# Optimization experiments

Measured on AMD Instinct MI355X. Metric: run time of the kernel, lower is better.

## Reference

```python
import jax, jax.numpy as jnp
import numpy as np

N_QUBITS = 12
N_LAYERS = 6
BATCH = 512
DIM = 2 ** N_QUBITS


def _apply_1q(psi, G, wire):
    """Apply a single-qubit gate on `wire` (wire 0 = most significant).
    psi: [B, 2^n] complex. G: [2,2] (shared) or [B,2,2] (batched)."""
    B = psi.shape[0]
    left = 2 ** wire
    psi = psi.reshape(B, left, 2, -1)
    if G.ndim == 2:
        psi = jnp.einsum('ij,bxjy->bxiy', G, psi)
    else:
        psi = jnp.einsum('bij,bxjy->bxiy', G, psi)
    return psi.reshape(B, -1)


def _apply_cnot(psi, c, t):
    """CNOT with control c, target t on [B, 2^n] state."""
    B = psi.shape[0]
    ps = psi.reshape((B,) + (2,) * N_QUBITS)
    ca, ta = c + 1, t + 1
    c0 = jnp.take(ps, 0, axis=ca)
    c1 = jnp.take(ps, 1, axis=ca)
    flip_ax = ta if ta < ca else ta - 1
    c1 = jnp.flip(c1, axis=flip_ax)  # X on target within control=1 block
    ps = jnp.stack([c0, c1], axis=ca)
    return ps.reshape(B, -1)


def _circuit(x, weights):
    B = x.shape[0]
    psi = jnp.zeros((B, DIM), jnp.complex64).at[:, 0].set(1.0)

    # AngleEmbedding: RY(x_w) on each wire (batched gate matrices)
    h = 0.5 * x
    c, s = jnp.cos(h).astype(jnp.complex64), jnp.sin(h).astype(jnp.complex64)
    for w in range(N_QUBITS):
        G = jnp.stack([jnp.stack([c[:, w], -s[:, w]], -1),
                       jnp.stack([s[:, w], c[:, w]], -1)], -2)  # [B,2,2]
        psi = _apply_1q(psi, G, w)

    # StronglyEntanglingLayers: Rot(phi,theta,omega) per wire, then ring of CNOTs
    for l in range(N_LAYERS):
        phi, theta, omega = weights[l, :, 0], weights[l, :, 1], weights[l, :, 2]
        ct = jnp.cos(0.5 * theta).astype(jnp.complex64)
        st = jnp.sin(0.5 * theta).astype(jnp.complex64)
        ep = jnp.exp(-0.5j * (phi + omega).astype(jnp.complex64))
        em = jnp.exp(0.5j * (phi - omega).astype(jnp.complex64))
        # Rot = RZ(omega) RY(theta) RZ(phi)
        m00 = ep * ct
        m01 = -em * st
        m10 = jnp.conj(em) * st
        m11 = jnp.conj(ep) * ct
        for w in range(N_QUBITS):
            G = jnp.array([[m00[w], m01[w]], [m10[w], m11[w]]], jnp.complex64)
            psi = _apply_1q(psi, G, w)
        r = l % (N_QUBITS - 1) + 1
        for w in range(N_QUBITS):
            psi = _apply_cnot(psi, w, (w + r) % N_QUBITS)

    # <Z_w> for every wire
    probs = psi.real ** 2 + psi.imag ** 2  # [B, 2^n]
    exps = []
    for w in range(N_QUBITS):
        p = probs.reshape(B, 2 ** w, 2, -1)
        exps.append(p[:, :, 0, :].sum((1, 2)) - p[:, :, 1, :].sum((1, 2)))
    return jnp.stack(exps, -1)  # [B, n_qubits]


def setup_inputs() -> dict:
    key = jax.random.key(0)
    k1, k2, k3, k4 = jax.random.split(key, 4)
    x = jax.random.uniform(k1, (BATCH, N_QUBITS), jnp.float32, -np.pi, np.pi)
    weights = jax.random.uniform(k2, (N_LAYERS, N_QUBITS, 3), jnp.float32, 0.0, 2.0 * np.pi)
    W = jax.random.normal(k3, (1, N_QUBITS), jnp.float32) * 0.3
    b = jax.random.normal(k4, (1,), jnp.float32) * 0.01
    return {"x": x, "weights": weights, "W": W, "b": b}


def reference(x, weights, W, b):
    z = _circuit(x, weights)              # [B, n_qubits]
    y = z @ W.T + b                       # [B, 1]
    return y.squeeze(-1)                  # [B]
```

## Files before the change

kernel.cpp:

```cpp
#include <hip/hip_runtime.h>
#include <stdint.h>

#define NQ 12
#define DIM 4096
#define NLAYERS 6
#define TPB 256

struct CK_t {
    uint32_t RC1[NLAYERS][NQ];
    uint32_t RC2[NQ];
    uint32_t RC3[NQ];
    uint32_t frow[NQ];
};

constexpr uint32_t G2f(uint32_t k){ return ((k&15u)<<8) | (k&0xF0u) | ((k>>8)&15u); }
constexpr uint32_t G3f(uint32_t k){ return ((k&15u)<<4) | ((k>>4)&15u) | (k&0xF00u); }
constexpr uint32_t Lstd(uint32_t k){ return ((k&15u)<<8) | (k>>4); }
constexpr uint32_t Lpr(uint32_t k){ return ((k>>6)&15u) | (((k>>4)&3u)<<4) | (((k>>10)&3u)<<6) | ((k&15u)<<8); }

constexpr CK_t build_ck() {
    CK_t ck{};
    uint32_t Acols[NLAYERS][NQ]{}, Aicol5[NQ]{};
    for (int l = 0; l < NLAYERS; l++) {
        int r = l % (NQ - 1) + 1;
        for (int q = 0; q < NQ; q++) {
            uint32_t v = 1u << q;
            for (int w = NQ - 1; w >= 0; w--) {
                int pc = NQ - 1 - w, pt = NQ - 1 - ((w + r) % NQ);
                v ^= ((v >> pc) & 1u) << pt;
            }
            Acols[l][q] = v;
            if (l == NLAYERS - 1) {
                uint32_t u = 1u << q;
                for (int w = 0; w < NQ; w++) {
                    int pc = NQ - 1 - w, pt = NQ - 1 - ((w + r) % NQ);
                    u ^= ((u >> pc) & 1u) << pt;
                }
                Aicol5[q] = u;
            }
        }
    }
    for (int j = 0; j < NQ; j++) ck.RC2[j] = Lstd(G2f(1u << j));
    for (int j = 0; j < NQ; j++) ck.RC3[j] = Lpr(G3f(1u << j));
    for (int l = 1; l < NLAYERS; l++)
        for (int j = 0; j < NQ; j++)
            ck.RC1[l][j] = Lstd(G3f(G2f(Acols[l - 1][j])));
    uint32_t Mcol[NQ]{};
    for (int j = 0; j < NQ; j++) {
        uint32_t pj = G2f(G3f(1u << j));
        uint32_t M = 0;
        for (int m = 0; m < NQ; m++) if ((pj >> m) & 1u) M ^= Aicol5[m];
        Mcol[j] = M;
    }
    for (int p = 0; p < NQ; p++) {
        uint32_t s = 0;
        for (int j = 0; j < NQ; j++) s |= ((Mcol[j] >> p) & 1u) << j;
        ck.frow[p] = s;
    }
    return ck;
}
constexpr CK_t CK = build_ck();

template<int KIND, int L, int PAR>
__device__ __forceinline__ void do_pass(float (&RE)[16], float (&IM)[16],
                                        float2* xb, int tid) {
    float2* buf = xb + PAR * DIM;
    int wbase;
    if constexpr (KIND == 3) wbase = (int)Lpr((uint32_t)tid << 4);
    else                     wbase = tid;
    #pragma unroll
    for (int l = 0; l < 16; l++)
        buf[wbase + (l << 8)] = make_float2(RE[l], IM[l]);

    uint32_t srcT = 0;
    #pragma unroll
    for (int j = 0; j < 8; j++) {
        uint32_t c = (KIND == 1) ? CK.RC1[L][4 + j]
                   : (KIND == 2) ? CK.RC2[4 + j] : CK.RC3[4 + j];
        srcT ^= ((tid >> j) & 1) ? c : 0u;
    }
    __syncthreads();
    #pragma unroll
    for (int l = 0; l < 16; l++) {
        uint32_t C = 0;
        #pragma unroll
        for (int q = 0; q < 4; q++)
            if ((l >> q) & 1)
                C ^= (KIND == 1) ? CK.RC1[L][q]
                   : (KIND == 2) ? CK.RC2[q] : CK.RC3[q];
        float2 v = buf[srcT ^ C];
        RE[l] = v.x; IM[l] = v.y;
    }
}

template<int L, int W, int Q>
__device__ __forceinline__ void reg_gate(float (&RE)[16], float (&IM)[16],
                                         const float4* smat) {
    float4 m = smat[L * NQ + W];
    #pragma unroll
    for (int l = 0; l < 16; l++) {
        if (l & (1 << Q)) continue;
        int l2 = l | (1 << Q);
        float a0r = RE[l], a0i = IM[l], a1r = RE[l2], a1i = IM[l2];
        RE[l]  = m.x * a0r - m.y * a0i + m.z * a1r - m.w * a1i;
        IM[l]  = m.x * a0i + m.y * a0r + m.z * a1i + m.w * a1r;
        RE[l2] = m.x * a1r + m.y * a1i - m.z * a0r - m.w * a0i;
        IM[l2] = m.x * a1i - m.y * a1r - m.z * a0i + m.w * a0r;
    }
}

template<int L>
__device__ __forceinline__ void do_layer(float (&RE)[16], float (&IM)[16],
                                         const float4* smat, float2* xb, int tid) {
    if constexpr (L > 0)
        do_pass<1, L, (3 * L - 1) & 1>(RE, IM, xb, tid);
    reg_gate<L, 11, 0>(RE, IM, smat);
    reg_gate<L, 10, 1>(RE, IM, smat);
    reg_gate<L,  9, 2>(RE, IM, smat);
    reg_gate<L,  8, 3>(RE, IM, smat);
    do_pass<2, L, (3 * L) & 1>(RE, IM, xb, tid);
    reg_gate<L, 3, 0>(RE, IM, smat);
    reg_gate<L, 2, 1>(RE, IM, smat);
    reg_gate<L, 1, 2>(RE, IM, smat);
    reg_gate<L, 0, 3>(RE, IM, smat);
    do_pass<3, L, (3 * L + 1) & 1>(RE, IM, xb, tid);
    reg_gate<L, 7, 0>(RE, IM, smat);
    reg_gate<L, 6, 1>(RE, IM, smat);
    reg_gate<L, 5, 2>(RE, IM, smat);
    reg_gate<L, 4, 3>(RE, IM, smat);
}

__global__ __launch_bounds__(TPB) void qsim_kernel(
    const float* __restrict__ x,
    const float* __restrict__ weights,
    const float* __restrict__ Wp,
    const float* __restrict__ bptr,
    float* __restrict__ out)
{
    __shared__ float2 xb[2 * DIM];
    __shared__ float4 smat[NLAYERS * NQ];
    __shared__ float  scs[NQ], sss[NQ];
    __shared__ float  red[4];

    const int tid = threadIdx.x;
    const int b   = blockIdx.x;

    if (tid < NQ) {
        float s_, c_;
        sincosf(0.5f * x[b * NQ + tid], &s_, &c_);
        scs[tid] = c_; sss[tid] = s_;
    }
    if (tid < NLAYERS * NQ) {
        float phi   = weights[tid * 3 + 0];
        float theta = weights[tid * 3 + 1];
        float omega = weights[tid * 3 + 2];
        float st, ct; sincosf(0.5f * theta, &st, &ct);
        float sp, cp; sincosf(0.5f * (phi + omega), &sp, &cp);
        float sm, cm; sincosf(0.5f * (phi - omega), &sm, &cm);
        smat[tid] = make_float4(cp * ct, -sp * ct, -cm * st, -sm * st);
    }
    __syncthreads();

    float base = 1.0f;
    #pragma unroll
    for (int p = 4; p < NQ; p++) {
        int w = NQ - 1 - p;
        base *= ((tid >> (p - 4)) & 1) ? sss[w] : scs[w];
    }
    float RE[16], IM[16];
    #pragma unroll
    for (int l = 0; l < 16; l++) {
        float a = base;
        #pragma unroll
        for (int p = 0; p < 4; p++) {
            int w = NQ - 1 - p;
            a *= ((l >> p) & 1) ? sss[w] : scs[w];
        }
        RE[l] = a; IM[l] = 0.0f;
    }

    do_layer<0>(RE, IM, smat, xb, tid);
    do_layer<1>(RE, IM, smat, xb, tid);
    do_layer<2>(RE, IM, smat, xb, tid);
    do_layer<3>(RE, IM, smat, xb, tid);
    do_layer<4>(RE, IM, smat, xb, tid);
    do_layer<5>(RE, IM, smat, xb, tid);

    const float bv = bptr[0];
    float wb[NQ];
    #pragma unroll
    for (int p = 0; p < NQ; p++) {
        uint32_t row = CK.frow[p];
        int tp = __popc(tid & (int)(row >> 4)) & 1;
        float Wv = Wp[NQ - 1 - p];
        wb[p] = tp ? -Wv : Wv;
    }
    float acc = 0.0f;
    #pragma unroll
    for (int l = 0; l < 16; l++) {
        float coef = bv;
        #pragma unroll
        for (int p = 0; p < NQ; p++)
            coef += (__popc(l & (int)(CK.frow[p] & 15u)) & 1) ? -wb[p] : wb[p];
        acc += (RE[l] * RE[l] + IM[l] * IM[l]) * coef;
    }
    #pragma unroll
    for (int off = 32; off > 0; off >>= 1)
        acc += __shfl_down(acc, off, 64);
    if ((tid & 63) == 0) red[tid >> 6] = acc;
    __syncthreads();
    if (tid == 0) out[b] = red[0] + red[1] + red[2] + red[3];
}

extern "C" void kernel_launch(void* const* d_in, const int* in_sizes, int n_in,
                              void* d_out, int out_size, void* d_ws, size_t ws_size,
                              hipStream_t stream) {
    const float* x       = (const float*)d_in[0];
    const float* weights = (const float*)d_in[1];
    const float* W       = (const float*)d_in[2];
    const float* bptr    = (const float*)d_in[3];
    qsim_kernel<<<512, TPB, 0, stream>>>(x, weights, W, bptr, (float*)d_out);
}
```

Measured before the change: 98.81 us.

## Compute conflict-avoiding shared-memory permutation layouts at compile time; pack complex as float2

Replaces the hand-written shared-memory index maps with layouts generated at compile time by a GF(2) basis search. The search picks write and read address bases so that wavefront accesses spread across LDS banks on both the store and the load side of each transpose pass. Thread address offsets for write and read are packed into a single XOR accumulation. It also stores amplitudes as two-wide float vectors so the gate math can use packed FP32 ops. The cost is a more complex constexpr construction and possibly different register allocation.

```diff
diff --git a/kernel.cpp b/kernel.cpp
--- a/kernel.cpp
+++ b/kernel.cpp
@@ -6,17 +6,91 @@
 #define NLAYERS 6
 #define TPB 256
 
+typedef float v2f __attribute__((ext_vector_type(2)));
+
+struct Pass_t {
+    uint32_t WT[8];
+    uint32_t WL[16];
+    uint32_t RT[8];
+    uint32_t RL[16];
+};
 struct CK_t {
-    uint32_t RC1[NLAYERS][NQ];
-    uint32_t RC2[NQ];
-    uint32_t RC3[NQ];
+    Pass_t PG2, PG3;
+    Pass_t P1[NLAYERS];
     uint32_t frow[NQ];
 };
 
 constexpr uint32_t G2f(uint32_t k){ return ((k&15u)<<8) | (k&0xF0u) | ((k>>8)&15u); }
 constexpr uint32_t G3f(uint32_t k){ return ((k&15u)<<4) | ((k>>4)&15u) | (k&0xF00u); }
-constexpr uint32_t Lstd(uint32_t k){ return ((k&15u)<<8) | (k>>4); }
-constexpr uint32_t Lpr(uint32_t k){ return ((k>>6)&15u) | (((k>>4)&3u)<<4) | (((k>>10)&3u)<<6) | ((k&15u)<<8); }
+
+constexpr uint32_t ech_reduce(const uint32_t* v, int n, uint32_t x){
+    bool ch = true;
+    while (ch) {
+        ch = false;
+        for (int i = 0; i < n; i++)
+            if (v[i] && (x ^ v[i]) < x) { x ^= v[i]; ch = true; }
+    }
+    return x;
+}
+
+constexpr Pass_t build_pass(const uint32_t* Mc) {
+    Pass_t P{};
+    uint32_t rows[12]{}; int nr = 0;
+    {
+        uint32_t e1[4]{}, e2[4]{}; int n1 = 0, n2 = 0;
+        for (int step = 0; step < 4; step++) {
+            bool found = false;
+            for (int pc = 1; pc <= 3 && !found; pc++) {
+                for (int a = 0; a < 12 && !found; a++)
+                for (int b = (pc >= 2 ? a + 1 : 12); (pc >= 2 ? b < 12 : b == 12) && !found; b++)
+                for (int c = (pc == 3 ? b + 1 : 12); (pc == 3 ? c < 12 : c == 12) && !found; c++) {
+                    uint32_t m = (1u << a);
+                    if (pc >= 2) m |= (1u << b);
+                    if (pc == 3) m |= (1u << c);
+                    uint32_t v1 = (m >> 4) & 15u;
+                    uint32_t v2 = 0;
+                    for (int j = 0; j < 4; j++)
+                        v2 |= (uint32_t)(__builtin_popcount(m & Mc[4 + j]) & 1) << j;
+                    uint32_t r1 = ech_reduce(e1, n1, v1);
+                    uint32_t r2 = ech_reduce(e2, n2, v2);
+                    if (r1 && r2) {
+                        rows[nr++] = m; e1[n1++] = r1; e2[n2++] = r2; found = true;
+                    }
+                }
+            }
+            if (!found) { rows[nr] = 1u << (4 + nr); nr++; }
+        }
+    }
+    {
+        uint32_t ef[12]{}; int nf = 0;
+        for (int i = 0; i < nr; i++) {
+            uint32_t r = ech_reduce(ef, nf, rows[i]);
+            if (r) ef[nf++] = r;
+        }
+        for (uint32_t m = 1; m < 4096u && nr < 12; m++) {
+            uint32_t r = ech_reduce(ef, nf, m);
+            if (r) { rows[nr++] = m; ef[nf++] = r; }
+        }
+    }
+    uint32_t col[12]{}, rc[12]{};
+    for (int j = 0; j < 12; j++) {
+        uint32_t c = 0;
+        for (int i = 0; i < 12; i++) c |= (uint32_t)((rows[i] >> j) & 1u) << i;
+        col[j] = c;
+    }
+    for (int j = 0; j < 12; j++) {
+        uint32_t a = 0, mc = Mc[j];
+        for (int q = 0; q < 12; q++) if ((mc >> q) & 1u) a ^= col[q];
+        rc[j] = a;
+    }
+    for (int j = 0; j < 8; j++) { P.WT[j] = col[4 + j]; P.RT[j] = rc[4 + j]; }
+    for (int l = 0; l < 16; l++) {
+        uint32_t aw = 0, ar = 0;
+        for (int q = 0; q < 4; q++) if ((l >> q) & 1) { aw ^= col[q]; ar ^= rc[q]; }
+        P.WL[l] = aw; P.RL[l] = ar;
+    }
+    return P;
+}
 
 constexpr CK_t build_ck() {
     CK_t ck{};
@@ -40,11 +114,14 @@
             }
         }
     }
-    for (int j = 0; j < NQ; j++) ck.RC2[j] = Lstd(G2f(1u << j));
-    for (int j = 0; j < NQ; j++) ck.RC3[j] = Lpr(G3f(1u << j));
-    for (int l = 1; l < NLAYERS; l++)
-        for (int j = 0; j < NQ; j++)
-            ck.RC1[l][j] = Lstd(G3f(G2f(Acols[l - 1][j])));
+    uint32_t McG2[12]{}, McG3[12]{}, Mc1[12]{};
+    for (int j = 0; j < 12; j++) { McG2[j] = G2f(1u << j); McG3[j] = G3f(1u << j); }
+    ck.PG2 = build_pass(McG2);
+    ck.PG3 = build_pass(McG3);
+    for (int l = 1; l < NLAYERS; l++) {
+        for (int j = 0; j < 12; j++) Mc1[j] = G3f(G2f(Acols[l - 1][j]));
+        ck.P1[l] = build_pass(Mc1);
+    }
     uint32_t Mcol[NQ]{};
     for (int j = 0; j < NQ; j++) {
         uint32_t pj = G2f(G3f(1u << j));
@@ -62,72 +139,59 @@
 constexpr CK_t CK = build_ck();
 
 template<int KIND, int L, int PAR>
-__device__ __forceinline__ void do_pass(float (&RE)[16], float (&IM)[16],
-                                        float2* xb, int tid) {
-    float2* buf = xb + PAR * DIM;
-    int wbase;
-    if constexpr (KIND == 3) wbase = (int)Lpr((uint32_t)tid << 4);
-    else                     wbase = tid;
+__device__ __forceinline__ void do_pass(v2f (&Z)[16], v2f* xb, int tid) {
+    constexpr Pass_t P = (KIND == 1) ? CK.P1[L] : (KIND == 2) ? CK.PG2 : CK.PG3;
+    v2f* buf = xb + PAR * DIM;
+    uint32_t comb = 0;
+    #pragma unroll
+    for (int j = 0; j < 8; j++) {
+        uint32_t pk = P.WT[j] | (P.RT[j] << 16);
+        comb ^= (uint32_t)(-(int)((tid >> j) & 1)) & pk;
+    }
+    uint32_t wbase = comb & 0xFFFu, rbase = comb >> 16;
     #pragma unroll
     for (int l = 0; l < 16; l++)
-        buf[wbase + (l << 8)] = make_float2(RE[l], IM[l]);
-
-    uint32_t srcT = 0;
-    #pragma unroll
-    for (int j = 0; j < 8; j++) {
-        uint32_t c = (KIND == 1) ? CK.RC1[L][4 + j]
-                   : (KIND == 2) ? CK.RC2[4 + j] : CK.RC3[4 + j];
-        srcT ^= ((tid >> j) & 1) ? c : 0u;
-    }
+        buf[wbase ^ P.WL[l]] = Z[l];
     __syncthreads();
     #pragma unroll
-    for (int l = 0; l < 16; l++) {
-        uint32_t C = 0;
-        #pragma unroll
-        for (int q = 0; q < 4; q++)
-            if ((l >> q) & 1)
-                C ^= (KIND == 1) ? CK.RC1[L][q]
-                   : (KIND == 2) ? CK.RC2[q] : CK.RC3[q];
-        float2 v = buf[srcT ^ C];
-        RE[l] = v.x; IM[l] = v.y;
-    }
+    for (int l = 0; l < 16; l++)
+        Z[l] = buf[rbase ^ P.RL[l]];
 }
 
 template<int L, int W, int Q>
-__device__ __forceinline__ void reg_gate(float (&RE)[16], float (&IM)[16],
-                                         const float4* smat) {
+__device__ __forceinline__ void reg_gate(v2f (&Z)[16], const float4* smat) {
     float4 m = smat[L * NQ + W];
     #pragma unroll
     for (int l = 0; l < 16; l++) {
         if (l & (1 << Q)) continue;
         int l2 = l | (1 << Q);
-        float a0r = RE[l], a0i = IM[l], a1r = RE[l2], a1i = IM[l2];
-        RE[l]  = m.x * a0r - m.y * a0i + m.z * a1r - m.w * a1i;
-        IM[l]  = m.x * a0i + m.y * a0r + m.z * a1i + m.w * a1r;
-        RE[l2] = m.x * a1r + m.y * a1i - m.z * a0r - m.w * a0i;
-        IM[l2] = m.x * a1i - m.y * a1r - m.z * a0i + m.w * a0r;
+        v2f z0 = Z[l], z1 = Z[l2];
+        v2f j0 = { -z0.y, z0.x };
+        v2f j1 = { -z1.y, z1.x };
+        Z[l]  = m.x * z0 + m.y * j0 + m.z * z1 + m.w * j1;
+        Z[l2] = m.x * z1 - m.y * j1 - m.z * z0 + m.w * j0;
     }
 }
 
 template<int L>
-__device__ __forceinline__ void do_layer(float (&RE)[16], float (&IM)[16],
-                                         const float4* smat, float2* xb, int tid) {
+__device__ __forceinline__ void do_layer(v2f (&Z)[16], const float4* smat,
+                                         v2f* xb, int tid) {
     if constexpr (L > 0)
-        do_pass<1, L, (3 * L - 1) & 1>(RE, IM, xb, tid);
-    reg_gate<L, 11, 0>(RE, IM, smat);
-    reg_gate<L, 10, 1>(RE, IM, smat);
-    reg_gate<L,  9, 2>(RE, IM, smat);
-    reg_gate<L,  8, 3>(RE, IM, smat);
-    do_pass<2, L, (3 * L) & 1>(RE, IM, xb, tid);
-    reg_gate<L, 3, 0>(RE, IM, smat);
-    reg_gate<L, 2, 1>(RE, IM, smat);
-    reg_gate<L, 1, 2>(RE, IM, smat);
-    reg_gate<L, 0, 3>(RE, IM, smat);
-    do_pass<3, L, (3 * L + 1) & 1>(RE, IM, xb, tid);
-    reg_gate<L, 7, 0>(RE, IM, smat);
-    reg_gate<L, 6, 1>(RE, IM, smat);
-    reg_gate<L, 5, 2>(RE, IM, smat);
-    reg_gate<L, 4, 3>(RE, IM, smat);
+        do_pass<1, L, (3 * L - 1) & 1>(Z, xb, tid);
+    reg_gate<L, 11, 0>(Z, smat);
+    reg_gate<L, 10, 1>(Z, smat);
+    reg_gate<L,  9, 2>(Z, smat);
+    reg_gate<L,  8, 3>(Z, smat);
+    do_pass<2, L, (3 * L) & 1>(Z, xb, tid);
+    reg_gate<L, 3, 0>(Z, smat);
+    reg_gate<L, 2, 1>(Z, smat);
+    reg_gate<L, 1, 2>(Z, smat);
+    reg_gate<L, 0, 3>(Z, smat);
+    do_pass<3, L, (3 * L + 1) & 1>(Z, xb, tid);
+    reg_gate<L, 7, 0>(Z, smat);
+    reg_gate<L, 6, 1>(Z, smat);
+    reg_gate<L, 5, 2>(Z, smat);
+    reg_gate<L, 4, 3>(Z, smat);
 }
 
 __global__ __launch_bounds__(TPB) void qsim_kernel(
@@ -137,7 +201,7 @@
     const float* __restrict__ bptr,
     float* __restrict__ out)
 {
-    __shared__ float2 xb[2 * DIM];
+    __shared__ v2f    xb[2 * DIM];
     __shared__ float4 smat[NLAYERS * NQ];
     __shared__ float  scs[NQ], sss[NQ];
     __shared__ float  red[4];
@@ -167,7 +231,7 @@
         int w = NQ - 1 - p;
         base *= ((tid >> (p - 4)) & 1) ? sss[w] : scs[w];
     }
-    float RE[16], IM[16];
+    v2f Z[16];
     #pragma unroll
     for (int l = 0; l < 16; l++) {
         float a = base;
@@ -176,15 +240,15 @@
             int w = NQ - 1 - p;
             a *= ((l >> p) & 1) ? sss[w] : scs[w];
         }
-        RE[l] = a; IM[l] = 0.0f;
-    }
-
-    do_layer<0>(RE, IM, smat, xb, tid);
-    do_layer<1>(RE, IM, smat, xb, tid);
-    do_layer<2>(RE, IM, smat, xb, tid);
-    do_layer<3>(RE, IM, smat, xb, tid);
-    do_layer<4>(RE, IM, smat, xb, tid);
-    do_layer<5>(RE, IM, smat, xb, tid);
+        Z[l].x = a; Z[l].y = 0.0f;
+    }
+
+    do_layer<0>(Z, smat, xb, tid);
+    do_layer<1>(Z, smat, xb, tid);
+    do_layer<2>(Z, smat, xb, tid);
+    do_layer<3>(Z, smat, xb, tid);
+    do_layer<4>(Z, smat, xb, tid);
+    do_layer<5>(Z, smat, xb, tid);
 
     const float bv = bptr[0];
     float wb[NQ];
@@ -202,7 +266,7 @@
         #pragma unroll
         for (int p = 0; p < NQ; p++)
             coef += (__popc(l & (int)(CK.frow[p] & 15u)) & 1) ? -wb[p] : wb[p];
-        acc += (RE[l] * RE[l] + IM[l] * IM[l]) * coef;
+        acc += (Z[l].x * Z[l].x + Z[l].y * Z[l].y) * coef;
     }
     #pragma unroll
     for (int off = 32; off > 0; off >>= 1)
```

After: 93.10 us. 5.8% less time.
